# Optimization experiments

Measured on AMD Instinct MI355X. Metric: run time of the kernel, lower is better.

The kernel has to match this reference:

```python
import jax, jax.numpy as jnp
import numpy as np

# Parsed from args.lbp_neighbor_offsets = "(-1,-1), (-1,0), (-1,1), (0,-1), (0,1), (1,-1), (1,0), (1,1)"
OFFSETS = [(-1, -1), (-1, 0), (-1, 1), (0, -1), (0, 1), (1, -1), (1, 0), (1, 1)]
MAX_OFF = 1  # max abs offset -> kernel_size=3, padding=1 (replicate)


def setup_inputs() -> dict:
    key = jax.random.key(0)
    img = jax.random.normal(key, (16, 1, 512, 512), dtype=jnp.float32)
    return {"img": img}


def reference(img):
    # img: [N, 1, H, W]
    # The torch conv kernel has exactly two nonzero taps per output channel:
    # +1 at (center+dy, center+dx) and -1 at center, with replicate padding.
    # Equivalent math: sigmoid(shift(img, (dy,dx), edge-replicate) - img).
    N, C, H, W = img.shape
    p = MAX_OFF
    padded = jnp.pad(img, ((0, 0), (0, 0), (p, p), (p, p)), mode='edge')
    # Fixed small loop over the 8 structurally distinct offsets (not a data dim).
    diffs = [padded[:, 0, p + dy:p + dy + H, p + dx:p + dx + W] - img[:, 0]
             for (dy, dx) in OFFSETS]
    # [N, num_neighbors, H, W]
    return jax.nn.sigmoid(jnp.stack(diffs, axis=1))
```

## Files before the change

### kernel.cpp

```cpp
#include <hip/hip_runtime.h>
#include <hip/hip_bf16.h>


#define LBP_N 16
#define LBP_H 512
#define LBP_W 512

__global__ __launch_bounds__(256) void lbp_kernel(const float* __restrict__ img,
                                                  float* __restrict__ out) {
    constexpr int H = LBP_H, W = LBP_W;
    int tid = blockIdx.x * blockDim.x + threadIdx.x;
    int w4 = tid & (W / 4 - 1);
    int h  = (tid >> 7) & (H - 1);
    int n  = tid >> 16;
    int w0 = w4 * 4;

    const float* src = img + (size_t)n * (H * W);
    int hm = max(h - 1, 0);
    int hp = min(h + 1, H - 1);

    float r0[6], r1[6], r2[6];
#pragma unroll
    for (int j = 0; j < 6; ++j) {
        int w = min(max(w0 + j - 1, 0), W - 1);
        r0[j] = src[hm * W + w];
        r1[j] = src[h  * W + w];
        r2[j] = src[hp * W + w];
    }

    float4 res[8];
#pragma unroll
    for (int i = 0; i < 4; ++i) {
        float c = r1[i + 1];
        float v[8] = { r0[i], r0[i + 1], r0[i + 2],
                       r1[i],            r1[i + 2],
                       r2[i], r2[i + 1], r2[i + 2] };
#pragma unroll
        for (int k = 0; k < 8; ++k) {
            float x = v[k] - c;
            float s = 1.0f / (1.0f + __expf(-x));
            reinterpret_cast<float*>(&res[k])[i] = s;
        }
    }

    float* dst = out + (size_t)n * (8 * H * W) + (size_t)h * W + w0;
#pragma unroll
    for (int k = 0; k < 8; ++k) {
        *reinterpret_cast<float4*>(dst + (size_t)k * (H * W)) = res[k];
    }
}

extern "C" void kernel_launch(void* const* d_in, const int* in_sizes, int n_in,
                              void* d_out, int out_size, void* d_ws, size_t ws_size,
                              hipStream_t stream) {
    const float* img = (const float*)d_in[0];
    float* out = (float*)d_out;
    int total = LBP_N * LBP_H * (LBP_W / 4);
    int block = 256;
    int grid = total / block;
    lbp_kernel<<<grid, block, 0, stream>>>(img, out);
}
```

Before: 30.84 us.

## Exploit sigmoid antisymmetry and compute 4x8 tile per thread

```diff
diff --git a/kernel.cpp b/kernel.cpp
--- a/kernel.cpp
+++ b/kernel.cpp
@@ -1,52 +1,109 @@
 #include <hip/hip_runtime.h>
-#include <hip/hip_bf16.h>
 
 
-#define LBP_N 16
-#define LBP_H 512
-#define LBP_W 512
+#define NH 512
+#define NW 512
+#define HWSZ (NH * NW)
 
-__global__ __launch_bounds__(256) void lbp_kernel(const float* __restrict__ img,
-                                                  float* __restrict__ out) {
-    constexpr int H = LBP_H, W = LBP_W;
-    int tid = blockIdx.x * blockDim.x + threadIdx.x;
-    int w4 = tid & (W / 4 - 1);
-    int h  = (tid >> 7) & (H - 1);
-    int n  = tid >> 16;
-    int w0 = w4 * 4;
+__device__ __forceinline__ float fexp2(float x) {
+#if __has_builtin(__builtin_amdgcn_exp2f)
+    return __builtin_amdgcn_exp2f(x);
+#else
+    return __expf(x * 0.6931471805599453f);
+#endif
+}
 
-    const float* src = img + (size_t)n * (H * W);
-    int hm = max(h - 1, 0);
-    int hp = min(h + 1, H - 1);
+__device__ __forceinline__ float sigm(float nbL, float cL) {
+    return __builtin_amdgcn_rcpf(1.0f + fexp2(cL - nbL));
+}
 
-    float r0[6], r1[6], r2[6];
+__global__ __launch_bounds__(256) void lbp_main(const float* __restrict__ img,
+                                                float* __restrict__ out) {
+    const float L2E = 1.4426950408889634f;
+    int t = blockIdx.x * 256 + threadIdx.x;
+    int lane = t & 63;
+    int w0 = lane << 3;
+    int strip = (t >> 6) & 127;
+    int h0 = strip << 2;
+    int n = t >> 13;
+
+    const float* src = img + (size_t)n * HWSZ;
+
+    float v[5][10];
+    int wl = max(w0 - 1, 0);
+    int wr = min(w0 + 8, NW - 1);
 #pragma unroll
-    for (int j = 0; j < 6; ++j) {
-        int w = min(max(w0 + j - 1, 0), W - 1);
-        r0[j] = src[hm * W + w];
-        r1[j] = src[h  * W + w];
-        r2[j] = src[hp * W + w];
+    for (int r = 0; r < 5; ++r) {
+        int row = max(h0 - 1 + r, 0);
+        const float* rp = src + row * NW;
+        float4 a = *reinterpret_cast<const float4*>(rp + w0);
+        float4 b = *reinterpret_cast<const float4*>(rp + w0 + 4);
+        v[r][0] = rp[wl] * L2E;
+        v[r][1] = a.x * L2E; v[r][2] = a.y * L2E; v[r][3] = a.z * L2E; v[r][4] = a.w * L2E;
+        v[r][5] = b.x * L2E; v[r][6] = b.y * L2E; v[r][7] = b.z * L2E; v[r][8] = b.w * L2E;
+        v[r][9] = rp[wr] * L2E;
     }
 
-    float4 res[8];
+    float* ob = out + (size_t)n * 8 * HWSZ;
+
 #pragma unroll
-    for (int i = 0; i < 4; ++i) {
-        float c = r1[i + 1];
-        float v[8] = { r0[i], r0[i + 1], r0[i + 2],
-                       r1[i],            r1[i + 2],
-                       r2[i], r2[i + 1], r2[i + 2] };
+    for (int k = 0; k < 4; ++k) {
+        const int dy = (k < 3) ? -1 : 0;
+        const int dx = (k == 0) ? -1 : (k == 1) ? 0 : (k == 2) ? 1 : -1;
+        float* odir = ob + (size_t)k * HWSZ;
+        float* oder = ob + (size_t)(7 - k) * HWSZ;
 #pragma unroll
-        for (int k = 0; k < 8; ++k) {
-            float x = v[k] - c;
-            float s = 1.0f / (1.0f + __expf(-x));
-            reinterpret_cast<float*>(&res[k])[i] = s;
+        for (int r = 0; r < 4; ++r) {
+            float s[8];
+#pragma unroll
+            for (int i = 0; i < 8; ++i)
+                s[i] = sigm(v[r + 1 + dy][i + 1 + dx], v[r + 1][i + 1]);
+
+            *reinterpret_cast<float4*>(odir + (h0 + r) * NW + w0) =
+                make_float4(s[0], s[1], s[2], s[3]);
+            *reinterpret_cast<float4*>(odir + (h0 + r) * NW + w0 + 4) =
+                make_float4(s[4], s[5], s[6], s[7]);
+
+            float vr8[8];
+            if (dx == -1) {
+#pragma unroll
+                for (int j = 0; j < 7; ++j) vr8[j] = 1.0f - s[j + 1];
+                vr8[7] = sigm(v[r + 1][9], v[r + 1 + dy][8]);
+            } else if (dx == 1) {
+                vr8[0] = sigm(v[r + 1][0], v[r][1]);
+#pragma unroll
+                for (int j = 1; j < 8; ++j) vr8[j] = 1.0f - s[j - 1];
+            } else {
+#pragma unroll
+                for (int j = 0; j < 8; ++j) vr8[j] = 1.0f - s[j];
+            }
+
+            int qrow = h0 + r + dy;
+            if (r > 0 || dy == 0 || h0 > 0) {
+                *reinterpret_cast<float4*>(oder + qrow * NW + w0) =
+                    make_float4(vr8[0], vr8[1], vr8[2], vr8[3]);
+                *reinterpret_cast<float4*>(oder + qrow * NW + w0 + 4) =
+                    make_float4(vr8[4], vr8[5], vr8[6], vr8[7]);
+            }
         }
     }
 
-    float* dst = out + (size_t)n * (8 * H * W) + (size_t)h * W + w0;
+    if (h0 == NH - 4) {
+        float e5[8], e7[8];
 #pragma unroll
-    for (int k = 0; k < 8; ++k) {
-        *reinterpret_cast<float4*>(dst + (size_t)k * (H * W)) = res[k];
+        for (int i = 0; i < 8; ++i) {
+            e7[i] = sigm(v[4][i + 2], v[4][i + 1]);
+            e5[i] = sigm(v[4][i], v[4][i + 1]);
+        }
+        float* o5 = ob + (size_t)5 * HWSZ + (NH - 1) * NW + w0;
+        float* o6 = ob + (size_t)6 * HWSZ + (NH - 1) * NW + w0;
+        float* o7 = ob + (size_t)7 * HWSZ + (NH - 1) * NW + w0;
+        *reinterpret_cast<float4*>(o5)     = make_float4(e5[0], e5[1], e5[2], e5[3]);
+        *reinterpret_cast<float4*>(o5 + 4) = make_float4(e5[4], e5[5], e5[6], e5[7]);
+        *reinterpret_cast<float4*>(o6)     = make_float4(0.5f, 0.5f, 0.5f, 0.5f);
+        *reinterpret_cast<float4*>(o6 + 4) = make_float4(0.5f, 0.5f, 0.5f, 0.5f);
+        *reinterpret_cast<float4*>(o7)     = make_float4(e7[0], e7[1], e7[2], e7[3]);
+        *reinterpret_cast<float4*>(o7 + 4) = make_float4(e7[4], e7[5], e7[6], e7[7]);
     }
 }
 
@@ -55,8 +112,5 @@
                               hipStream_t stream) {
     const float* img = (const float*)d_in[0];
     float* out = (float*)d_out;
-    int total = LBP_N * LBP_H * (LBP_W / 4);
-    int block = 256;
-    int grid = total / block;
-    lbp_kernel<<<grid, block, 0, stream>>>(img, out);
+    lbp_main<<<512, 256, 0, stream>>>(img, out);
 }
```

New measurement: 32.33 us. 4.8% more time.
